# Kernel optimization log

Hardware: AMD Instinct MI355X
Metric: run time of the kernel (lower is better)

## Reference

```python
import jax, jax.numpy as jnp
import numpy as np

GRID = 14  # encoded_image_size

def _grid_edge_index():
    # Exact replica of build_adjacency_matrix().nonzero(): 8-neighbor 14x14 grid.
    edges = []
    for r in range(GRID):
        for c in range(GRID):
            i = r * GRID + c
            for rr in range(max(0, r - 1), min(r + 2, GRID)):
                for cc in range(max(0, c - 1), min(c + 2, GRID)):
                    if rr == r and cc == c:
                        continue
                    edges.append((i, rr * GRID + cc))
    return np.asarray(edges, dtype=np.int64).T  # (2, 1404)


def setup_inputs() -> dict:
    key = jax.random.key(0)
    k1, k2, k3 = jax.random.split(key, 3)
    B, H, W, C, Hid = 128, 14, 14, 2048, 1024
    x = jax.random.normal(k1, (B, H, W, C), dtype=jnp.float32)
    edge_index = jnp.asarray(_grid_edge_index())
    W1 = jax.random.normal(k2, (C, Hid), dtype=jnp.float32) * (1.0 / np.sqrt(C))
    b1 = jnp.zeros((Hid,), jnp.float32)
    W2 = jax.random.normal(k3, (Hid, C), dtype=jnp.float32) * (1.0 / np.sqrt(Hid))
    b2 = jnp.zeros((C,), jnp.float32)
    return {"x": x, "edge_index": edge_index, "W1": W1, "b1": b1, "W2": W2, "b2": b2}


def _gcn_conv(h, W, b, src, dst, dinv):
    # PyG GCNConv: linear transform, symmetric deg-normalized (A+I) aggregation, bias.
    h = h @ W  # [N, out]
    norm = (dinv[src] * dinv[dst])[:, None]
    agg = jax.ops.segment_sum(h[src] * norm, dst, num_segments=h.shape[0])
    agg = agg + h * (dinv * dinv)[:, None]  # self-loop term, norm = 1/deg_i
    return agg + b


def reference(x, edge_index, W1, b1, W2, b2):
    B, H, Wd, C = x.shape
    N = B * H * Wd
    # Faithful to original: permute(0,3,1,2) then reshape(-1, C) (layout-scrambling).
    xf = jnp.transpose(x, (0, 3, 1, 2)).reshape(-1, C)  # [N, C]
    src, dst = edge_index[0], edge_index[1]
    # Degrees over ALL N nodes: self-loop (=1) everywhere + incoming grid edges
    # (only first 196 nodes have grid neighbors; rest are passthrough).
    deg = jnp.ones((N,), xf.dtype).at[dst].add(1.0)
    dinv = jax.lax.rsqrt(deg)
    h = jax.nn.relu(_gcn_conv(xf, W1, b1, src, dst, dinv))
    h = jax.nn.relu(_gcn_conv(h, W2, b2, src, dst, dinv))
    # reshape + permute(0,3,1,2) + permute(0,2,3,1) == identity back to NHWC.
    return h.reshape(B, H, Wd, C)
```

## Files before the change

kernel.cpp:

```cpp
#include <hip/hip_runtime.h>

typedef float  float4_t __attribute__((ext_vector_type(4)));
typedef __bf16 bf16x8   __attribute__((ext_vector_type(8)));

#define BM 256
#define BN 128
#define BK 32

#define GLD16(g, l)                                                        \
    __builtin_amdgcn_global_load_lds(                                      \
        (const __attribute__((address_space(1))) void*)(g),                \
        (__attribute__((address_space(3))) void*)(l), 16, 0, 0)

__global__ __launch_bounds__(256)
void transpose_x_kernel(const float* __restrict__ x, __bf16* __restrict__ A1)
{
    __shared__ float sm[32 * 221];
    const int b  = blockIdx.y;
    const int c0 = blockIdx.x * 32;
    const int t  = threadIdx.x;

    const float* xb = x + (size_t)b * 401408;
    const int c4 = (t & 7) * 4;
    const int p0 = t >> 3;
#pragma unroll
    for (int k = 0; k < 7; ++k) {
        int p = p0 + k * 32;
        if (p < 196) {
            float4_t v = *(const float4_t*)&xb[(size_t)p * 2048 + c0 + c4];
#pragma unroll
            for (int i = 0; i < 4; ++i)
                sm[(c4 + i) * 221 + p + (p >> 3)] = v[i];
        }
    }
    __syncthreads();

    __bf16* ab = A1 + (size_t)b * 401408 + (size_t)c0 * 196;
#pragma unroll
    for (int k = 0; k < 4; ++k) {
        int o8 = k * 256 + t;
        if (o8 < 784) {
            int o  = o8 * 8;
            int cc = o / 196;
            int pp = o - cc * 196;
            bf16x8 v;
#pragma unroll
            for (int i = 0; i < 8; ++i) {
                v[i] = (__bf16)sm[cc * 221 + pp + (pp >> 3)];
                if (++pp == 196) { pp = 0; ++cc; }
            }
            *(bf16x8*)(ab + o) = v;
        }
    }
}

__global__ void transpose_w_kernel(const float* __restrict__ W, __bf16* __restrict__ Wt,
                                   int K, int N)
{
    __shared__ float tile[32][33];
    const int kt = blockIdx.x * 32, nt = blockIdx.y * 32;
    const int tx = threadIdx.x, ty = threadIdx.y;
#pragma unroll
    for (int rr = 0; rr < 4; ++rr)
        tile[ty + rr * 8][tx] = W[(size_t)(kt + ty + rr * 8) * N + nt + tx];
    __syncthreads();
#pragma unroll
    for (int rr = 0; rr < 4; ++rr)
        Wt[(size_t)(nt + ty + rr * 8) * K + kt + tx] = (__bf16)tile[tx][ty + rr * 8];
}

template<bool OUT_BF16, int LNX>
__global__ __launch_bounds__(256, 2)
void gemm_bt_kernel(const __bf16* __restrict__ A,
                    const __bf16* __restrict__ Bt,
                    const float* __restrict__ bias,
                    void* __restrict__ out,
                    float* __restrict__ raw_out,
                    int M, int N, int K)
{
    __shared__ __bf16 lds[3 * 12288];

    const int tid  = threadIdx.x;
    const int wid  = tid >> 6;
    const int lane = tid & 63;

    const int lid  = blockIdx.x + gridDim.x * blockIdx.y;
    const int xcd  = lid & 7;
    const int i0   = lid >> 3;
    const int ni   = i0 & ((1 << LNX) - 1);
    const int mseq = i0 >> LNX;
    const int mi   = (mseq << 3) + xcd;
    const int row0 = mi * BM;
    if (row0 >= M) return;
    const int col0 = ni * BN;

    const int wave_m = (wid >> 1) * 128;
    const int wave_n = (wid & 1) * 64;

    float4_t acc[8][4];
#pragma unroll
    for (int i = 0; i < 8; ++i)
#pragma unroll
        for (int j = 0; j < 4; ++j)
            acc[i][j] = (float4_t){0.f, 0.f, 0.f, 0.f};

    const int    stg_row = (wid << 4) + ((lane >> 3) << 1) + ((lane >> 2) & 1);
    const int    stg_k   = (((lane & 3) ^ ((lane >> 3) & 3)) << 3);
    const int    wb      = wid << 9;
    const __bf16* gA     = A  + (size_t)(row0 + stg_row) * K + stg_k;
    const __bf16* gB     = Bt + (size_t)(col0 + stg_row) * K + stg_k;

#define STAGE(t, d) do {                                       \
    const __bf16* ga = gA + (size_t)(t) * BK;                  \
    const __bf16* gb = gB + (size_t)(t) * BK;                  \
    GLD16(ga,                    (d) +         wb);            \
    GLD16(ga +  64 * (size_t)K,  (d) + 2048  + wb);            \
    GLD16(ga + 128 * (size_t)K,  (d) + 4096  + wb);            \
    GLD16(ga + 192 * (size_t)K,  (d) + 6144  + wb);            \
    GLD16(gb,                    (d) + 8192  + wb);            \
    GLD16(gb +  64 * (size_t)K,  (d) + 10240 + wb);            \
} while (0)

    STAGE(0, lds);
    STAGE(1, lds + 12288);
    asm volatile("s_waitcnt vmcnt(6)" ::: "memory");
    __builtin_amdgcn_s_barrier();
    __builtin_amdgcn_sched_barrier(0);

    const int slotf   = ((lane & 1) << 2) + ((lane >> 4) ^ ((lane >> 1) & 3));
    const int la_base = ((wave_m >> 1) + ((lane & 15) >> 1)) * 64 + slotf * 8;
    const int lb_base = 8192 + ((wave_n >> 1) + ((lane & 15) >> 1)) * 64 + slotf * 8;

    const int NTt = K / BK;
    int cur = 0, st2 = 2;
    for (int t = 0; t < NTt; ++t) {
        const __bf16* cA = lds + cur * 12288;
        __bf16* dst = lds + st2 * 12288;
        const bool do_stage = (t < NTt - 2);

        bf16x8 af[8], bfr[4];
#pragma unroll
        for (int i = 0; i < 8; ++i)
            af[i] = *(const bf16x8*)&cA[la_base + i * 512];
#pragma unroll
        for (int j = 0; j < 4; ++j)
            bfr[j] = *(const bf16x8*)&cA[lb_base + j * 512];
        if (do_stage) STAGE(t + 2, dst);

        __builtin_amdgcn_s_setprio(1);
#pragma unroll
        for (int i = 0; i < 8; ++i)
#pragma unroll
            for (int j = 0; j < 4; ++j)
                acc[i][j] = __builtin_amdgcn_mfma_f32_16x16x32_bf16(
                    af[i], bfr[j], acc[i][j], 0, 0, 0);
        __builtin_amdgcn_s_setprio(0);

        if (t < NTt - 1) {
            asm volatile("s_waitcnt lgkmcnt(0)" ::: "memory");
            if (do_stage) asm volatile("s_waitcnt vmcnt(6)" ::: "memory");
            else          asm volatile("s_waitcnt vmcnt(0)" ::: "memory");
            __builtin_amdgcn_s_barrier();
            __builtin_amdgcn_sched_barrier(0);
        }
        cur = (cur == 2) ? 0 : cur + 1;
        st2 = (st2 == 2) ? 0 : st2 + 1;
    }
#undef STAGE

    const int crow = (lane >> 4) * 4;
    const int ccol = lane & 15;
    const bool has_raw = (row0 == 0);
#pragma unroll
    for (int i = 0; i < 8; ++i) {
#pragma unroll
        for (int j = 0; j < 4; ++j) {
            int gcol = col0 + wave_n + j * 16 + ccol;
            float bv = bias[gcol];
#pragma unroll
            for (int r = 0; r < 4; ++r) {
                int grow = row0 + wave_m + i * 16 + crow + r;
                float v = acc[i][j][r];
                if (has_raw && grow < 196) raw_out[grow * N + gcol] = v;
                float o = fmaxf(v + bv, 0.f);
                if (OUT_BF16) ((__bf16*)out)[(size_t)grow * N + gcol] = (__bf16)o;
                else          ((float*)out)[(size_t)grow * N + gcol] = o;
            }
        }
    }
}

template<typename OutT>
__global__ void fixup_kernel(const float* __restrict__ raw, const float* __restrict__ bias,
                             OutT* __restrict__ out, int N)
{
    const int q = blockIdx.x;
    const int r = q / 14, c = q % 14;
    int nbr[8];
    int cnt = 0;
    for (int rr = (r > 0 ? r - 1 : 0); rr <= (r < 13 ? r + 1 : 13); ++rr)
        for (int cc = (c > 0 ? c - 1 : 0); cc <= (c < 13 ? c + 1 : 13); ++cc)
            if (!(rr == r && cc == c)) nbr[cnt++] = rr * 14 + cc;
    const float dq    = 1.f / sqrtf(1.f + (float)cnt);
    const float wself = 1.f / (1.f + (float)cnt);
    float wn[8];
    for (int t = 0; t < cnt; ++t) {
        int pr = nbr[t] / 14, pc = nbr[t] % 14;
        int pcnt = ((pr < 13 ? pr + 1 : 13) - (pr > 0 ? pr - 1 : 0) + 1) *
                   ((pc < 13 ? pc + 1 : 13) - (pc > 0 ? pc - 1 : 0) + 1) - 1;
        wn[t] = dq / sqrtf(1.f + (float)pcnt);
    }
    const int ch = blockIdx.y * 256 + threadIdx.x;
    float s = raw[q * N + ch] * wself;
    for (int t = 0; t < cnt; ++t) s += raw[nbr[t] * N + ch] * wn[t];
    float o = fmaxf(s + bias[ch], 0.f);
    out[(size_t)q * N + ch] = (OutT)o;
}

extern "C" void kernel_launch(void* const* d_in, const int* in_sizes, int n_in,
                              void* d_out, int out_size, void* d_ws, size_t ws_size,
                              hipStream_t stream)
{
    const float* x  = (const float*)d_in[0];
    const float* W1 = (const float*)d_in[2];
    const float* b1 = (const float*)d_in[3];
    const float* W2 = (const float*)d_in[4];
    const float* b2 = (const float*)d_in[5];

    const int M = 25088, C = 2048, Hid = 1024;

    __bf16* A1 = (__bf16*)d_out;

    char* ws = (char*)d_ws;
    __bf16* A2    = (__bf16*)(ws);
    __bf16* W1t   = (__bf16*)(ws + 51380224);
    __bf16* W2t   = (__bf16*)(ws + 55574528);
    float*  h1raw = (float*)(ws + 59768832);
    float*  h2raw = (float*)(ws + 60571648);

    transpose_x_kernel<<<dim3(64, 128), 256, 0, stream>>>(x, A1);
    transpose_w_kernel<<<dim3(C / 32, Hid / 32), dim3(32, 8), 0, stream>>>(W1, W1t, C, Hid);
    transpose_w_kernel<<<dim3(Hid / 32, C / 32), dim3(32, 8), 0, stream>>>(W2, W2t, Hid, C);

    gemm_bt_kernel<true, 3><<<dim3(Hid / BN, 104), 256, 0, stream>>>(
        A1, W1t, b1, (void*)A2, h1raw, M, Hid, C);
    fixup_kernel<__bf16><<<dim3(196, Hid / 256), 256, 0, stream>>>(h1raw, b1, A2, Hid);

    gemm_bt_kernel<false, 4><<<dim3(C / BN, 104), 256, 0, stream>>>(
        A2, W2t, b2, d_out, h2raw, M, C, Hid);
    fixup_kernel<float><<<dim3(196, C / 256), 256, 0, stream>>>(h2raw, b2, (float*)d_out, C);
}
```

Before: 608.9 us.

## Switch GEMM to 256x256x64 tiles with 8 waves and phased LDS pipeline

Enlarges the GEMM block tile to 256x256 with BK=64 and 512 threads (8 waves), double-buffering LDS instead of triple-buffering. Each k-step is split into four compute phases, and the global-to-LDS loads for the next tile are spread across them, with barriers between phases. The aim is more MFMA work per byte loaded and better overlap of loads with compute. The cost is more barriers per k-step, 128 KB of LDS per block (which may limit residency), and fewer blocks in the grid.

```diff
diff --git a/kernel.cpp b/kernel.cpp
--- a/kernel.cpp
+++ b/kernel.cpp
@@ -4,8 +4,8 @@
 typedef __bf16 bf16x8   __attribute__((ext_vector_type(8)));
 
 #define BM 256
-#define BN 128
-#define BK 32
+#define BN 256
+#define BK 64
 
 #define GLD16(g, l)                                                        \
     __builtin_amdgcn_global_load_lds(                                      \
@@ -70,7 +70,7 @@
 }
 
 template<bool OUT_BF16, int LNX>
-__global__ __launch_bounds__(256, 2)
+__global__ __launch_bounds__(512, 2)
 void gemm_bt_kernel(const __bf16* __restrict__ A,
                     const __bf16* __restrict__ Bt,
                     const float* __restrict__ bias,
@@ -78,7 +78,7 @@
                     float* __restrict__ raw_out,
                     int M, int N, int K)
 {
-    __shared__ __bf16 lds[3 * 12288];
+    __shared__ __bf16 lds[2 * 32768];
 
     const int tid  = threadIdx.x;
     const int wid  = tid >> 6;
@@ -94,8 +94,8 @@
     if (row0 >= M) return;
     const int col0 = ni * BN;
 
-    const int wave_m = (wid >> 1) * 128;
-    const int wave_n = (wid & 1) * 64;
+    const int wave_m = (wid >> 2) * 128;
+    const int wave_n = (wid & 3) * 64;
 
     float4_t acc[8][4];
 #pragma unroll
@@ -104,69 +104,108 @@
         for (int j = 0; j < 4; ++j)
             acc[i][j] = (float4_t){0.f, 0.f, 0.f, 0.f};
 
-    const int    stg_row = (wid << 4) + ((lane >> 3) << 1) + ((lane >> 2) & 1);
-    const int    stg_k   = (((lane & 3) ^ ((lane >> 3) & 3)) << 3);
-    const int    wb      = wid << 9;
-    const __bf16* gA     = A  + (size_t)(row0 + stg_row) * K + stg_k;
-    const __bf16* gB     = Bt + (size_t)(col0 + stg_row) * K + stg_k;
-
-#define STAGE(t, d) do {                                       \
-    const __bf16* ga = gA + (size_t)(t) * BK;                  \
-    const __bf16* gb = gB + (size_t)(t) * BK;                  \
-    GLD16(ga,                    (d) +         wb);            \
-    GLD16(ga +  64 * (size_t)K,  (d) + 2048  + wb);            \
-    GLD16(ga + 128 * (size_t)K,  (d) + 4096  + wb);            \
-    GLD16(ga + 192 * (size_t)K,  (d) + 6144  + wb);            \
-    GLD16(gb,                    (d) + 8192  + wb);            \
-    GLD16(gb +  64 * (size_t)K,  (d) + 10240 + wb);            \
-} while (0)
-
-    STAGE(0, lds);
-    STAGE(1, lds + 12288);
-    asm volatile("s_waitcnt vmcnt(6)" ::: "memory");
+    const int    srow = (wid << 3) + (lane >> 3);
+    const int    scol = ((lane & 7) ^ (lane >> 3)) << 3;
+    const int    wdst = wid << 9;
+    const __bf16* gA  = A  + (size_t)(row0 + srow) * K + scol;
+    const __bf16* gB  = Bt + (size_t)(col0 + srow) * K + scol;
+
+#define AS(s, ko, d) GLD16(gA + (size_t)(s) * 64 * K + (ko), (d) + (s) * 4096 + wdst)
+#define BS(s, ko, d) GLD16(gB + (size_t)(s) * 64 * K + (ko), (d) + 16384 + (s) * 4096 + wdst)
+
+    AS(0, 0, lds); AS(1, 0, lds); AS(2, 0, lds); AS(3, 0, lds);
+    BS(0, 0, lds); BS(1, 0, lds); BS(2, 0, lds); BS(3, 0, lds);
+    asm volatile("s_waitcnt vmcnt(0)" ::: "memory");
     __builtin_amdgcn_s_barrier();
     __builtin_amdgcn_sched_barrier(0);
 
-    const int slotf   = ((lane & 1) << 2) + ((lane >> 4) ^ ((lane >> 1) & 3));
-    const int la_base = ((wave_m >> 1) + ((lane & 15) >> 1)) * 64 + slotf * 8;
-    const int lb_base = 8192 + ((wave_n >> 1) + ((lane & 15) >> 1)) * 64 + slotf * 8;
-
-    const int NTt = K / BK;
-    int cur = 0, st2 = 2;
-    for (int t = 0; t < NTt; ++t) {
-        const __bf16* cA = lds + cur * 12288;
-        __bf16* dst = lds + st2 * 12288;
-        const bool do_stage = (t < NTt - 2);
-
-        bf16x8 af[8], bfr[4];
-#pragma unroll
-        for (int i = 0; i < 8; ++i)
-            af[i] = *(const bf16x8*)&cA[la_base + i * 512];
-#pragma unroll
-        for (int j = 0; j < 4; ++j)
-            bfr[j] = *(const bf16x8*)&cA[lb_base + j * 512];
-        if (do_stage) STAGE(t + 2, dst);
-
-        __builtin_amdgcn_s_setprio(1);
-#pragma unroll
-        for (int i = 0; i < 8; ++i)
+    const int m15  = lane & 15;
+    const int q    = lane >> 4;
+    const int l7   = lane & 7;
+    const int swz0 = ((q) ^ l7) << 3;
+    const int swz1 = ((4 + q) ^ l7) << 3;
+    const int arow = (wave_m + m15) * 64;
+    const int brow = 16384 + (wave_n + m15) * 64;
+
+#define PHASE_SYNC()                                            \
+    __builtin_amdgcn_s_barrier();                               \
+    asm volatile("s_waitcnt lgkmcnt(0)" ::: "memory");          \
+    __builtin_amdgcn_sched_barrier(0)
+
+    const int NTt = K >> 6;
+    for (int kt = 0; kt < NTt; ++kt) {
+        const __bf16* cA  = lds + (kt & 1) * 32768;
+        __bf16*       dst = lds + ((kt + 1) & 1) * 32768;
+        const bool    st  = (kt < NTt - 1);
+        const size_t  ko  = (size_t)(kt + 1) * 64;
+
+        bf16x8 bfr[4], afA[4], afB[4];
+
+#pragma unroll
+        for (int j = 0; j < 4; ++j) bfr[j] = *(const bf16x8*)&cA[brow + j * 1024 + swz0];
+#pragma unroll
+        for (int i = 0; i < 4; ++i) afA[i] = *(const bf16x8*)&cA[arow + i * 1024 + swz0];
+        if (st) { AS(0, ko, dst); AS(1, ko, dst); AS(2, ko, dst); }
+        PHASE_SYNC();
+        __builtin_amdgcn_s_setprio(1);
+#pragma unroll
+        for (int i = 0; i < 4; ++i)
 #pragma unroll
             for (int j = 0; j < 4; ++j)
                 acc[i][j] = __builtin_amdgcn_mfma_f32_16x16x32_bf16(
-                    af[i], bfr[j], acc[i][j], 0, 0, 0);
-        __builtin_amdgcn_s_setprio(0);
-
-        if (t < NTt - 1) {
-            asm volatile("s_waitcnt lgkmcnt(0)" ::: "memory");
-            if (do_stage) asm volatile("s_waitcnt vmcnt(6)" ::: "memory");
-            else          asm volatile("s_waitcnt vmcnt(0)" ::: "memory");
-            __builtin_amdgcn_s_barrier();
-            __builtin_amdgcn_sched_barrier(0);
-        }
-        cur = (cur == 2) ? 0 : cur + 1;
-        st2 = (st2 == 2) ? 0 : st2 + 1;
-    }
-#undef STAGE
+                    afA[i], bfr[j], acc[i][j], 0, 0, 0);
+        __builtin_amdgcn_s_setprio(0);
+        __builtin_amdgcn_s_barrier();
+
+#pragma unroll
+        for (int i = 0; i < 4; ++i) afB[i] = *(const bf16x8*)&cA[arow + (i + 4) * 1024 + swz0];
+        if (st) { AS(3, ko, dst); BS(0, ko, dst); BS(1, ko, dst); }
+        PHASE_SYNC();
+        __builtin_amdgcn_s_setprio(1);
+#pragma unroll
+        for (int i = 0; i < 4; ++i)
+#pragma unroll
+            for (int j = 0; j < 4; ++j)
+                acc[i + 4][j] = __builtin_amdgcn_mfma_f32_16x16x32_bf16(
+                    afB[i], bfr[j], acc[i + 4][j], 0, 0, 0);
+        __builtin_amdgcn_s_setprio(0);
+        __builtin_amdgcn_s_barrier();
+
+#pragma unroll
+        for (int j = 0; j < 4; ++j) bfr[j] = *(const bf16x8*)&cA[brow + j * 1024 + swz1];
+#pragma unroll
+        for (int i = 0; i < 4; ++i) afA[i] = *(const bf16x8*)&cA[arow + i * 1024 + swz1];
+        if (st) { BS(2, ko, dst); BS(3, ko, dst); }
+        PHASE_SYNC();
+        __builtin_amdgcn_s_setprio(1);
+#pragma unroll
+        for (int i = 0; i < 4; ++i)
+#pragma unroll
+            for (int j = 0; j < 4; ++j)
+                acc[i][j] = __builtin_amdgcn_mfma_f32_16x16x32_bf16(
+                    afA[i], bfr[j], acc[i][j], 0, 0, 0);
+        __builtin_amdgcn_s_setprio(0);
+        __builtin_amdgcn_s_barrier();
+
+#pragma unroll
+        for (int i = 0; i < 4; ++i) afB[i] = *(const bf16x8*)&cA[arow + (i + 4) * 1024 + swz1];
+        PHASE_SYNC();
+        __builtin_amdgcn_s_setprio(1);
+#pragma unroll
+        for (int i = 0; i < 4; ++i)
+#pragma unroll
+            for (int j = 0; j < 4; ++j)
+                acc[i + 4][j] = __builtin_amdgcn_mfma_f32_16x16x32_bf16(
+                    afB[i], bfr[j], acc[i + 4][j], 0, 0, 0);
+        __builtin_amdgcn_s_setprio(0);
+        __builtin_amdgcn_sched_barrier(0);
+        if (st) asm volatile("s_waitcnt vmcnt(0)" ::: "memory");
+        __builtin_amdgcn_s_barrier();
+        __builtin_amdgcn_sched_barrier(0);
+    }
+#undef AS
+#undef BS
+#undef PHASE_SYNC
 
     const int crow = (lane >> 4) * 4;
     const int ccol = lane & 15;
@@ -242,11 +281,11 @@
     transpose_w_kernel<<<dim3(C / 32, Hid / 32), dim3(32, 8), 0, stream>>>(W1, W1t, C, Hid);
     transpose_w_kernel<<<dim3(Hid / 32, C / 32), dim3(32, 8), 0, stream>>>(W2, W2t, Hid, C);
 
-    gemm_bt_kernel<true, 3><<<dim3(Hid / BN, 104), 256, 0, stream>>>(
+    gemm_bt_kernel<true, 2><<<dim3(Hid / BN, 104), 512, 0, stream>>>(
         A1, W1t, b1, (void*)A2, h1raw, M, Hid, C);
     fixup_kernel<__bf16><<<dim3(196, Hid / 256), 256, 0, stream>>>(h1raw, b1, A2, Hid);
 
-    gemm_bt_kernel<false, 4><<<dim3(C / BN, 104), 256, 0, stream>>>(
+    gemm_bt_kernel<false, 3><<<dim3(C / BN, 104), 512, 0, stream>>>(
         A2, W2t, b2, d_out, h2raw, M, C, Hid);
     fixup_kernel<float><<<dim3(196, C / 256), 256, 0, stream>>>(h2raw, b2, (float*)d_out, C);
 }
```

Result: slower. 629.9 us (+3.5%).
